# Kernel tuning notes

Measured on AMD Instinct MI355X. Metric: run time of the kernel, lower is better.

## Reference

```python
import jax, jax.numpy as jnp
import numpy as np

B = 4096       # batch
D = 256        # num_features
H = 512        # proposal_hidden_units
K = 10         # mixture_components
C = 64         # context_units
L = 4          # proposal_residual_blocks
S = 10         # num_importance_samples (call default)
HEAD = 3 * K + C
LOG2PI = float(np.log(2.0 * np.pi))


def setup_inputs() -> dict:
    key = jax.random.key(0)
    ks = jax.random.split(key, 10)
    x = jax.random.normal(ks[0], (B, D), jnp.float32)
    observed_mask = (jax.random.uniform(ks[1], (B, D)) < 0.5).astype(jnp.float32)
    s_in = 1.0 / np.sqrt(2 * D)
    s_h = 1.0 / np.sqrt(H)
    W_in = (jax.random.normal(ks[2], (2 * D, H), jnp.float32) * s_in)
    b_in = jnp.zeros((H,), jnp.float32)
    W1 = jax.random.normal(ks[3], (L, H, H), jnp.float32) * s_h
    b1 = jnp.zeros((L, H), jnp.float32)
    W2 = jax.random.normal(ks[4], (L, H, H), jnp.float32) * s_h
    b2 = jnp.zeros((L, H), jnp.float32)
    W_fin = jax.random.normal(ks[5], (H, D * HEAD), jnp.float32) * s_h
    b_fin = jnp.zeros((D * HEAD,), jnp.float32)
    return {
        "x": x, "observed_mask": observed_mask,
        "W_in": W_in, "b_in": b_in,
        "W1": W1, "b1": b1, "W2": W2, "b2": b2,
        "W_fin": W_fin, "b_fin": b_fin,
        "num_importance_samples": S,
    }


def _proposal_params(x_o, observed_mask, W_in, b_in, W1, b1, W2, b2, W_fin, b_fin):
    # Residual MLP proposal network on [x_o, observed_mask].
    h = jnp.concatenate([x_o, observed_mask], axis=-1) @ W_in + b_in  # [B, H]
    for l in range(L):
        r = jax.nn.relu(h) @ W1[l] + b1[l]
        r = jax.nn.relu(r) @ W2[l] + b2[l]
        h = h + r
    out = (h @ W_fin + b_fin).reshape(h.shape[0], D, HEAD)  # [B, D, 3K+C]
    logits = out[..., :K]
    means = out[..., K:2 * K]
    scales = jax.nn.softplus(out[..., 2 * K:3 * K]) + 1e-3
    return logits, means, scales


def reference(x, observed_mask, W_in, b_in, W1, b1, W2, b2, W_fin, b_fin,
              num_importance_samples):
    query = 1.0 - observed_mask
    x_o = x * observed_mask
    x_u = x * query

    logits, means, scales = _proposal_params(
        x_o, observed_mask, W_in, b_in, W1, b1, W2, b2, W_fin, b_fin)

    # Per-feature mixture-of-Gaussians log-likelihood of x_u, masked by query.
    log_w = jax.nn.log_softmax(logits, axis=-1)               # [B, D, K]
    z = (x_u[..., None] - means) / scales
    comp_ll = -0.5 * z * z - jnp.log(scales) - 0.5 * LOG2PI   # [B, D, K]
    proposal_ll = jax.scipy.special.logsumexp(log_w + comp_ll, axis=-1) * query

    # Samples (stop_gradient in the original).
    skey = jax.random.key(1234)
    kc, kn = jax.random.split(skey)
    comp = jax.random.categorical(kc, logits, axis=-1,
                                  shape=(num_importance_samples,) + logits.shape[:2])  # [S, B, D]
    mu = jnp.take_along_axis(means[None], comp[..., None], axis=-1)[..., 0]    # [S, B, D]
    sg = jnp.take_along_axis(scales[None], comp[..., None], axis=-1)[..., 0]   # [S, B, D]
    eps = jax.random.normal(kn, comp.shape, jnp.float32)
    samples = mu + sg * eps                                   # [S, B, D]
    samples = jnp.transpose(samples, (1, 0, 2))               # [B, S, D]
    samples = jax.lax.stop_gradient(samples) * query[:, None, :]
    # call() multiplies by query twice (before and after selected_features block)
    proposal_samples = samples * query[:, None, :]

    proposal_mean = jnp.sum(jax.nn.softmax(logits, axis=-1) * means, axis=-1) * query
    proposal_mean = proposal_mean * query  # second masking, as in call()

    return proposal_ll, proposal_samples, proposal_mean
```

## Files before the change

### kernel.cpp

```cpp
#include <hip/hip_runtime.h>
#include <cstdint>

#define B 4096
#define D 256
#define H 512
#define K 10
#define NL 4
#define S 10
#define NOUT 30
#define HEADW 94
#define ND (B*D)
#define NFIN 7680
#define NLOG 2560
#define NMS  5120

typedef __bf16 bf16x8 __attribute__((ext_vector_type(8)));
typedef float  f32x16 __attribute__((ext_vector_type(16)));

__host__ __device__ inline void threefry2x32(uint32_t k0, uint32_t k1,
                                             uint32_t x0, uint32_t x1,
                                             uint32_t& o0, uint32_t& o1) {
  uint32_t ks2 = k0 ^ k1 ^ 0x1BD11BDAu;
#define TF_ROT(x, r) (((x) << (r)) | ((x) >> (32 - (r))))
#define TF_RND(r) { x0 += x1; x1 = TF_ROT(x1, r); x1 ^= x0; }
  x0 += k0; x1 += k1;
  TF_RND(13) TF_RND(15) TF_RND(26) TF_RND(6)
  x0 += k1; x1 += ks2 + 1u;
  TF_RND(17) TF_RND(29) TF_RND(16) TF_RND(24)
  x0 += ks2; x1 += k0 + 2u;
  TF_RND(13) TF_RND(15) TF_RND(26) TF_RND(6)
  x0 += k0; x1 += k1 + 3u;
  TF_RND(17) TF_RND(29) TF_RND(16) TF_RND(24)
  x0 += k1; x1 += ks2 + 4u;
  TF_RND(13) TF_RND(15) TF_RND(26) TF_RND(6)
  x0 += ks2; x1 += k0 + 5u;
  o0 = x0; o1 = x1;
#undef TF_RND
#undef TF_ROT
}

__device__ __forceinline__ uint32_t rb32(uint32_t k0, uint32_t k1, uint32_t idx) {
  uint32_t a, b;
  threefry2x32(k0, k1, 0u, idx, a, b);
  return a ^ b;
}

__device__ __forceinline__ float u01_from_bits(uint32_t bits) {
  return __uint_as_float((bits >> 9) | 0x3f800000u) - 1.0f;
}

__device__ __forceinline__ float erfinv_f32(float x) {
  float w = -log1pf(-x * x);
  float p;
  if (w < 5.0f) {
    w = w - 2.5f;
    p = 2.81022636e-08f;
    p = fmaf(p, w, 3.43273939e-07f);
    p = fmaf(p, w, -3.5233877e-06f);
    p = fmaf(p, w, -4.39150654e-06f);
    p = fmaf(p, w, 0.00021858087f);
    p = fmaf(p, w, -0.00125372503f);
    p = fmaf(p, w, -0.00417768164f);
    p = fmaf(p, w, 0.246640727f);
    p = fmaf(p, w, 1.50140941f);
  } else {
    w = sqrtf(w) - 3.0f;
    p = -0.000200214257f;
    p = fmaf(p, w, 0.000100950558f);
    p = fmaf(p, w, 0.00134934322f);
    p = fmaf(p, w, -0.00367342844f);
    p = fmaf(p, w, 0.00573950773f);
    p = fmaf(p, w, -0.0076224613f);
    p = fmaf(p, w, 0.00943887047f);
    p = fmaf(p, w, 1.00167406f);
    p = fmaf(p, w, 2.83297682f);
  }
  return p * x;
}

__device__ __forceinline__ unsigned short bf16_rne(float x) {
  uint32_t u = __float_as_uint(x);
  uint32_t r = u + 0x7fffu + ((u >> 16) & 1u);
  return (unsigned short)(r >> 16);
}

__device__ __forceinline__ void split2(float x, short& hi, short& lo) {
  unsigned short hb = bf16_rne(x);
  float hf = __uint_as_float((uint32_t)hb << 16);
  hi = (short)hb;
  lo = (short)bf16_rne(x - hf);
}

__device__ __forceinline__ void gload16(const void* g, void* l) {
  __builtin_amdgcn_global_load_lds(
      (const __attribute__((address_space(1))) void*)g,
      (__attribute__((address_space(3))) void*)l, 16, 0, 0);
}

__global__ __launch_bounds__(256) void prep_kernel(const float* __restrict__ x,
                                                   const float* __restrict__ mask,
                                                   float* __restrict__ xcat) {
  int i = blockIdx.x * 256 + threadIdx.x;
  if (i >= B * 2 * D) return;
  int b = i >> 9, c = i & 511;
  float v = (c < D) ? x[b * D + c] * mask[b * D + c] : mask[b * D + (c - D)];
  xcat[i] = v;
}

__global__ __launch_bounds__(256) void wgatherL(const float* __restrict__ Wf,
                                                float* __restrict__ wsgL) {
  int c = blockIdx.x * 256 + threadIdx.x;
  int k = blockIdx.y;
  int dd = c / K, j = c - dd * K;
  wsgL[(size_t)k * NLOG + c] = Wf[(size_t)k * (D * HEADW) + dd * HEADW + j];
}

__global__ __launch_bounds__(256) void wsplit_ms(const float* __restrict__ Wf,
                                                 short* __restrict__ whi,
                                                 short* __restrict__ wlo) {
  __shared__ float tile[32][33];
  int n0 = blockIdx.x * 32, k0 = blockIdx.y * 32;
  int tx = threadIdx.x & 31, ty = threadIdx.x >> 5;
#pragma unroll
  for (int r = 0; r < 4; ++r) {
    int k = k0 + ty + r * 8;
    int n = n0 + tx;
    int dd = n / 20, j = n - dd * 20;
    tile[ty + r * 8][tx] = Wf[(size_t)k * (D * HEADW) + dd * HEADW + 10 + j];
  }
  __syncthreads();
#pragma unroll
  for (int r = 0; r < 4; ++r) {
    int n = n0 + ty + r * 8;
    int k = k0 + tx;
    float v = tile[tx][ty + r * 8];
    short hb, lb;
    split2(v, hb, lb);
    int nb = n >> 7, nl = n & 127;
    int kc = k >> 5, sub = (k >> 4) & 1, kh = (k >> 3) & 1, e = k & 7;
    size_t idx = ((((size_t)(nb * 16 + kc) * 4 + sub * 2 + kh) * 128 + nl) * 8) + e;
    whi[idx] = hb;
    wlo[idx] = lb;
  }
}

template <int RELU, int RES>
__global__ __launch_bounds__(256) void gemm_trunk(const float* __restrict__ A,
                                                  const float* __restrict__ W,
                                                  const float* __restrict__ bias,
                                                  const float* res, float* C) {
  __shared__ float As[64 * 68];
  __shared__ float Ws[64 * 64];
  const int tid = threadIdx.x;
  const int lane = tid & 63, wid = tid >> 6;
  const int tx = tid & 15, ty = tid >> 4;
  const int bm = blockIdx.y * 64, bn = blockIdx.x * 64;
  const int ls = tid & 15, lm = tid >> 4;

  float acc[4][4] = {};

  for (int k0 = 0; k0 < H; k0 += 64) {
#pragma unroll
    for (int c = wid; c < 16; c += 4) {
      gload16(W + (size_t)(k0 + c * 4 + (lane >> 4)) * H + bn + (lane & 15) * 4,
              Ws + c * 256 + lane * 4);
    }
#pragma unroll
    for (int r = 0; r < 4; ++r) {
      int m = lm + 16 * r;
      float4 f = *(const float4*)(A + (size_t)(bm + m) * H + k0 + 4 * ls);
      if (RELU) {
        f.x = fmaxf(f.x, 0.0f); f.y = fmaxf(f.y, 0.0f);
        f.z = fmaxf(f.z, 0.0f); f.w = fmaxf(f.w, 0.0f);
      }
      As[(4 * ls + 0) * 68 + m] = f.x;
      As[(4 * ls + 1) * 68 + m] = f.y;
      As[(4 * ls + 2) * 68 + m] = f.z;
      As[(4 * ls + 3) * 68 + m] = f.w;
    }
    __syncthreads();
#pragma unroll
    for (int kk = 0; kk < 64; ++kk) {
      float4 a4 = *(const float4*)(As + kk * 68 + ty * 4);
      float4 b4 = *(const float4*)(Ws + kk * 64 + tx * 4);
      float a[4] = {a4.x, a4.y, a4.z, a4.w};
      float b[4] = {b4.x, b4.y, b4.z, b4.w};
#pragma unroll
      for (int i = 0; i < 4; ++i)
#pragma unroll
        for (int j = 0; j < 4; ++j) acc[i][j] = fmaf(a[i], b[j], acc[i][j]);
    }
    __syncthreads();
  }
#pragma unroll
  for (int i = 0; i < 4; ++i) {
    int row = bm + ty * 4 + i;
#pragma unroll
    for (int j = 0; j < 4; ++j) {
      int col = bn + tx * 4 + j;
      float v = acc[i][j] + bias[col];
      if (RES) v = res[(size_t)row * H + col] + v;
      C[(size_t)row * H + col] = v;
    }
  }
}

__global__ __launch_bounds__(256) void gemm_head(const float* __restrict__ A,
                                                 const float* __restrict__ Wg,
                                                 const short* __restrict__ Bh,
                                                 const short* __restrict__ Bl,
                                                 const float* __restrict__ bf,
                                                 const float* __restrict__ msk,
                                                 float* __restrict__ headout) {
  __shared__ __align__(16) float smem[8448];
  const int tid = threadIdx.x;
  const int lane = tid & 63, wid = tid >> 6;
  const int bm = blockIdx.y * 128;

  if (blockIdx.x < 20) {
    float* As = smem;
    float* Ws = smem + 4352;
    const int tx = tid & 15, ty = tid >> 4;
    const int bn = blockIdx.x * 128;
    const int ls = tid & 7, lm = tid >> 3;

    float acc[8][8] = {};

    for (int k0 = 0; k0 < H; k0 += 32) {
#pragma unroll
      for (int c = wid; c < 16; c += 4) {
        gload16(Wg + (size_t)(k0 + c * 2 + (lane >> 5)) * NLOG + bn + (lane & 31) * 4,
                Ws + c * 256 + lane * 4);
      }
#pragma unroll
      for (int r = 0; r < 4; ++r) {
        int m = lm + 32 * r;
        float4 f = *(const float4*)(A + (size_t)(bm + m) * H + k0 + 4 * ls);
        As[(4 * ls + 0) * 136 + m] = f.x;
        As[(4 * ls + 1) * 136 + m] = f.y;
        As[(4 * ls + 2) * 136 + m] = f.z;
        As[(4 * ls + 3) * 136 + m] = f.w;
      }
      __syncthreads();
#pragma unroll
      for (int kk = 0; kk < 32; ++kk) {
        float a[8], b[8];
        *(float4*)(a + 0) = *(const float4*)(As + kk * 136 + ty * 8);
        *(float4*)(a + 4) = *(const float4*)(As + kk * 136 + ty * 8 + 4);
        *(float4*)(b + 0) = *(const float4*)(Ws + kk * 128 + tx * 4);
        *(float4*)(b + 4) = *(const float4*)(Ws + kk * 128 + 64 + tx * 4);
#pragma unroll
        for (int i = 0; i < 8; ++i)
#pragma unroll
          for (int j = 0; j < 8; ++j) acc[i][j] = fmaf(a[i], b[j], acc[i][j]);
      }
      __syncthreads();
    }
#pragma unroll
    for (int i = 0; i < 8; ++i) {
      int row = bm + ty * 8 + i;
#pragma unroll
      for (int j = 0; j < 8; ++j) {
        int c = bn + ((j < 4) ? (tx * 4 + j) : (64 + tx * 4 + (j - 4)));
        int dd = c / K, jj = c - dd * K;
        if (msk[(size_t)row * D + dd] != 0.0f) continue;
        float v = acc[i][j] + bf[dd * HEADW + jj];
        headout[(size_t)row * NFIN + dd * NOUT + jj] = v;
      }
    }
  } else {
    short* lds = (short*)smem;
    const int wm = wid >> 1, wn = wid & 1;
    const int nb = blockIdx.x - 20;
    const int ls = tid & 7, lm = tid >> 3;

    short* ldsAh = lds;
    short* ldsAl = lds + 4096;
    short* ldsBh = lds + 8192;
    short* ldsBl = lds + 12288;

    const short* gBh = Bh + (size_t)nb * 65536;
    const short* gBl = Bl + (size_t)nb * 65536;

    f32x16 acc[2][2];
#pragma unroll
    for (int mt = 0; mt < 2; ++mt)
#pragma unroll
      for (int nt = 0; nt < 2; ++nt)
#pragma unroll
        for (int i = 0; i < 16; ++i) acc[mt][nt][i] = 0.0f;

    for (int kc = 0; kc < 16; ++kc) {
      const short* cBh = gBh + kc * 4096;
      const short* cBl = gBl + kc * 4096;
#pragma unroll
      for (int c = wid; c < 8; c += 4) {
        gload16(cBh + c * 512 + lane * 8, ldsBh + c * 512);
        gload16(cBl + c * 512 + lane * 8, ldsBl + c * 512);
      }
      int k0 = kc * 32;
#pragma unroll
      for (int r = 0; r < 4; ++r) {
        int m = lm + 32 * r;
        float4 f = *(const float4*)(A + (size_t)(bm + m) * H + k0 + 4 * ls);
        short4 h4, l4;
        split2(f.x, h4.x, l4.x); split2(f.y, h4.y, l4.y);
        split2(f.z, h4.z, l4.z); split2(f.w, h4.w, l4.w);
        int off = ((((ls >> 2) * 2 + ((ls >> 1) & 1)) * 128 + m) * 8) + (ls & 1) * 4;
        *(short4*)(ldsAh + off) = h4;
        *(short4*)(ldsAl + off) = l4;
      }
      __syncthreads();
#pragma unroll
      for (int sub = 0; sub < 2; ++sub) {
        bf16x8 ah[2], al[2], bh[2], bl[2];
#pragma unroll
        for (int mt = 0; mt < 2; ++mt) {
          int r = wm * 64 + mt * 32 + (lane & 31);
          int off = ((sub * 2 + (lane >> 5)) * 128 + r) * 8;
          ah[mt] = *(const bf16x8*)(ldsAh + off);
          al[mt] = *(const bf16x8*)(ldsAl + off);
        }
#pragma unroll
        for (int nt = 0; nt < 2; ++nt) {
          int r = wn * 64 + nt * 32 + (lane & 31);
          int off = ((sub * 2 + (lane >> 5)) * 128 + r) * 8;
          bh[nt] = *(const bf16x8*)(ldsBh + off);
          bl[nt] = *(const bf16x8*)(ldsBl + off);
        }
#pragma unroll
        for (int mt = 0; mt < 2; ++mt)
#pragma unroll
          for (int nt = 0; nt < 2; ++nt) {
            acc[mt][nt] = __builtin_amdgcn_mfma_f32_32x32x16_bf16(ah[mt], bh[nt], acc[mt][nt], 0, 0, 0);
            acc[mt][nt] = __builtin_amdgcn_mfma_f32_32x32x16_bf16(ah[mt], bl[nt], acc[mt][nt], 0, 0, 0);
            acc[mt][nt] = __builtin_amdgcn_mfma_f32_32x32x16_bf16(al[mt], bh[nt], acc[mt][nt], 0, 0, 0);
          }
      }
      __syncthreads();
    }

#pragma unroll
    for (int mt = 0; mt < 2; ++mt)
#pragma unroll
      for (int nt = 0; nt < 2; ++nt) {
        int col = nb * 128 + wn * 64 + nt * 32 + (lane & 31);
        int rbase = bm + wm * 64 + mt * 32 + 4 * (lane >> 5);
        int dd = col / 20, j = col - dd * 20;
#pragma unroll
        for (int reg = 0; reg < 16; ++reg) {
          int row = rbase + (reg & 3) + 8 * (reg >> 2);
          if (msk[(size_t)row * D + dd] != 0.0f) continue;
          float v = acc[mt][nt][reg] + bf[dd * HEADW + 10 + j];
          if (j >= 10) v = (fmaxf(v, 0.0f) + log1pf(expf(-fabsf(v)))) + 0.001f;
          headout[(size_t)row * NFIN + dd * NOUT + 10 + j] = v;
        }
      }
  }
}

__global__ __launch_bounds__(256) void init_counter(int* counter) {
  if (threadIdx.x == 0 && blockIdx.x == 0) *counter = 0;
}

__global__ __launch_bounds__(256) void compact_zero(const float* __restrict__ mask,
                                                    float* __restrict__ out_ll,
                                                    float* __restrict__ out_s,
                                                    float* __restrict__ out_mean,
                                                    int* __restrict__ list,
                                                    int* __restrict__ counter) {
  int idx = blockIdx.x * 256 + threadIdx.x;
  if (idx >= ND) return;
  if (mask[idx] != 0.0f) {
    int b = idx >> 8, d = idx & (D - 1);
    out_ll[idx] = 0.0f;
    out_mean[idx] = 0.0f;
#pragma unroll
    for (int s = 0; s < S; ++s) out_s[((size_t)b * S + s) * D + d] = 0.0f;
  } else {
    int pos = atomicAdd(counter, 1);
    list[pos] = idx;
  }
}

__global__ __launch_bounds__(256) void fused_tail(const float* __restrict__ head,
                                                  const float* __restrict__ x,
                                                  const float* __restrict__ mask,
                                                  const int* __restrict__ list,
                                                  const int* __restrict__ counter,
                                                  float* __restrict__ out_ll,
                                                  float* __restrict__ out_s,
                                                  float* __restrict__ out_mean,
                                                  uint32_t kc0, uint32_t kc1,
                                                  uint32_t kn0, uint32_t kn1) {
  int i = blockIdx.x * 256 + threadIdx.x;
  if (i >= *counter) return;
  int idx = list[i];
  int b = idx >> 8, d = idx & (D - 1);
  const float* hp = head + (size_t)idx * NOUT;
  float lg[K], mn[K], sc[K];
#pragma unroll
  for (int k = 0; k < K; ++k) { lg[k] = hp[k]; mn[k] = hp[K + k]; sc[k] = hp[2 * K + k]; }
  float q = 1.0f - mask[idx];
  float xu = x[idx] * q;
  float m = lg[0];
#pragma unroll
  for (int k = 1; k < K; ++k) m = fmaxf(m, lg[k]);
  float e[K];
  float sum = 0.0f;
#pragma unroll
  for (int k = 0; k < K; ++k) { e[k] = expf(lg[k] - m); sum += e[k]; }
  float lse = logf(sum);
  float a[K];
  float amax = -3.402823466e38f;
#pragma unroll
  for (int k = 0; k < K; ++k) {
    float z = (xu - mn[k]) / sc[k];
    float cll = -0.5f * z * z - logf(sc[k]) - 0.9189385332046727f;
    float lw = (lg[k] - m) - lse;
    a[k] = lw + cll;
    amax = fmaxf(amax, a[k]);
  }
  float s2 = 0.0f;
#pragma unroll
  for (int k = 0; k < K; ++k) s2 += expf(a[k] - amax);
  out_ll[idx] = (logf(s2) + amax) * q;
  float pm = 0.0f;
#pragma unroll
  for (int k = 0; k < K; ++k) pm += (e[k] / sum) * mn[k];
  out_mean[idx] = pm * q;
  float inv_e[K];
#pragma unroll
  for (int k = 0; k < K; ++k) inv_e[k] = 1.0f / e[k];
  for (int s = 0; s < S; ++s) {
    uint32_t t32 = (uint32_t)s * (uint32_t)ND + (uint32_t)idx;
    uint32_t base = t32 * (uint32_t)K;
    int best = 0;
    float rbest = 3.402823466e38f;
#pragma unroll
    for (int k = 0; k < K; ++k) {
      uint32_t bits = rb32(kc0, kc1, base + (uint32_t)k);
      float u = u01_from_bits(bits);
      float wv = -__log2f(u);
      float r = wv * inv_e[k];
      if (r < rbest) { rbest = r; best = k; }
    }
    uint32_t ebits = rb32(kn0, kn1, t32);
    float f = u01_from_bits(ebits);
    float r2 = f * 2.0f + (-0.99999994f);
    r2 = fmaxf(r2, -0.99999994f);
    float eps = 1.4142135623730951f * erfinv_f32(r2);
    out_s[((size_t)b * S + s) * D + d] = (mn[best] + sc[best] * eps) * q;
  }
}

extern "C" void kernel_launch(void* const* d_in, const int* in_sizes, int n_in,
                              void* d_out, int out_size, void* d_ws, size_t ws_size,
                              hipStream_t stream) {
  const float* x    = (const float*)d_in[0];
  const float* mask = (const float*)d_in[1];
  const float* W_in = (const float*)d_in[2];
  const float* b_in = (const float*)d_in[3];
  const float* W1   = (const float*)d_in[4];
  const float* b1   = (const float*)d_in[5];
  const float* W2   = (const float*)d_in[6];
  const float* b2   = (const float*)d_in[7];
  const float* Wf   = (const float*)d_in[8];
  const float* bf   = (const float*)d_in[9];

  char* w = (char*)d_ws;
  float* head   = (float*)w;
  float* xcat   = head;
  float* t      = head;
  float* h      = (float*)(w + 125829120);
  float* wsgL   = (float*)(w + 134217728);
  int*   list   = (int*)(w + 134217728);
  short* wms_h  = (short*)(w + 139460608);
  short* wms_l  = (short*)(w + 144703488);
  int*   counter = (int*)(w + 149946368);

  float* out_ll   = (float*)d_out;
  float* out_s    = out_ll + (size_t)ND;
  float* out_mean = out_s + (size_t)ND * S;

  wgatherL<<<dim3(NLOG / 256, 512), 256, 0, stream>>>(Wf, wsgL);
  wsplit_ms<<<dim3(NMS / 32, 512 / 32), 256, 0, stream>>>(Wf, wms_h, wms_l);

  prep_kernel<<<(B * 2 * D) / 256, 256, 0, stream>>>(x, mask, xcat);

  dim3 gtr(H / 64, B / 64);
  gemm_trunk<0, 0><<<gtr, 256, 0, stream>>>(xcat, W_in, b_in, nullptr, h);
  for (int l = 0; l < NL; ++l) {
    gemm_trunk<1, 0><<<gtr, 256, 0, stream>>>(h, W1 + (size_t)l * H * H,
                                              b1 + (size_t)l * H, nullptr, t);
    gemm_trunk<1, 1><<<gtr, 256, 0, stream>>>(t, W2 + (size_t)l * H * H,
                                              b2 + (size_t)l * H, h, h);
  }

  gemm_head<<<dim3(60, B / 128), 256, 0, stream>>>(h, wsgL, wms_h, wms_l, bf,
                                                   mask, head);

  init_counter<<<1, 256, 0, stream>>>(counter);
  compact_zero<<<ND / 256, 256, 0, stream>>>(mask, out_ll, out_s, out_mean,
                                             list, counter);

  uint32_t kc0, kc1, kn0, kn1;
  threefry2x32(0u, 1234u, 0u, 0u, kc0, kc1);
  threefry2x32(0u, 1234u, 0u, 1u, kn0, kn1);
  fused_tail<<<ND / 256, 256, 0, stream>>>(head, x, mask, list, counter,
                                           out_ll, out_s, out_mean,
                                           kc0, kc1, kn0, kn1);
}
```

Measured before the change: 1.314 ms.

## Double-buffer LDS staging in MFMA head GEMM and drop mask-based store skipping

The bf16-split MFMA path of the head GEMM now double-buffers its LDS tiles, staging chunk kc+1 while computing chunk kc with a single barrier per iteration, and uses a simpler A-tile layout with packed 128-bit stores. The aim is to hide global-load and split latency behind MFMA work. Shared memory doubles to 64KB per block, which may lower occupancy. The per-element mask check before writing head outputs is also removed, so every head value is written, trading more stores for less branching and fewer mask loads.

```diff
diff --git a/kernel.cpp b/kernel.cpp
--- a/kernel.cpp
+++ b/kernel.cpp
@@ -91,6 +91,10 @@
   lo = (short)bf16_rne(x - hf);
 }
 
+__device__ __forceinline__ uint32_t pk2(short a, short b) {
+  return (uint32_t)(uint16_t)a | ((uint32_t)(uint16_t)b << 16);
+}
+
 __device__ __forceinline__ void gload16(const void* g, void* l) {
   __builtin_amdgcn_global_load_lds(
       (const __attribute__((address_space(1))) void*)g,
@@ -205,14 +209,41 @@
   }
 }
 
+__device__ __forceinline__ void stage_ms(short* ls0, const float* Ab,
+                                         const short* gBh, const short* gBl,
+                                         int kc, int tid) {
+  const short* cBh = gBh + kc * 4096;
+  const short* cBl = gBl + kc * 4096;
+  gload16(cBh + tid * 8,        ls0 + 8192 + tid * 8);
+  gload16(cBh + 2048 + tid * 8, ls0 + 10240 + tid * 8);
+  gload16(cBl + tid * 8,        ls0 + 12288 + tid * 8);
+  gload16(cBl + 2048 + tid * 8, ls0 + 14336 + tid * 8);
+#pragma unroll
+  for (int p = 0; p < 2; ++p) {
+    int u = tid + p * 256;
+    int slot = u >> 7, row = u & 127;
+    const float* ap = Ab + (size_t)row * 512 + kc * 32 + slot * 8;
+    float4 f0 = *(const float4*)ap;
+    float4 f1 = *(const float4*)(ap + 4);
+    short h0,h1,h2,h3,h4,h5,h6,h7, l0,l1,l2,l3,l4,l5,l6,l7;
+    split2(f0.x, h0, l0); split2(f0.y, h1, l1);
+    split2(f0.z, h2, l2); split2(f0.w, h3, l3);
+    split2(f1.x, h4, l4); split2(f1.y, h5, l5);
+    split2(f1.z, h6, l6); split2(f1.w, h7, l7);
+    uint4 hv = { pk2(h0,h1), pk2(h2,h3), pk2(h4,h5), pk2(h6,h7) };
+    uint4 lv = { pk2(l0,l1), pk2(l2,l3), pk2(l4,l5), pk2(l6,l7) };
+    *(uint4*)(ls0 + u * 8)        = hv;
+    *(uint4*)(ls0 + 4096 + u * 8) = lv;
+  }
+}
+
 __global__ __launch_bounds__(256) void gemm_head(const float* __restrict__ A,
                                                  const float* __restrict__ Wg,
                                                  const short* __restrict__ Bh,
                                                  const short* __restrict__ Bl,
                                                  const float* __restrict__ bf,
-                                                 const float* __restrict__ msk,
                                                  float* __restrict__ headout) {
-  __shared__ __align__(16) float smem[8448];
+  __shared__ __align__(16) float smem[16384];
   const int tid = threadIdx.x;
   const int lane = tid & 63, wid = tid >> 6;
   const int bm = blockIdx.y * 128;
@@ -263,7 +294,6 @@
       for (int j = 0; j < 8; ++j) {
         int c = bn + ((j < 4) ? (tx * 4 + j) : (64 + tx * 4 + (j - 4)));
         int dd = c / K, jj = c - dd * K;
-        if (msk[(size_t)row * D + dd] != 0.0f) continue;
         float v = acc[i][j] + bf[dd * HEADW + jj];
         headout[(size_t)row * NFIN + dd * NOUT + jj] = v;
       }
@@ -272,15 +302,10 @@
     short* lds = (short*)smem;
     const int wm = wid >> 1, wn = wid & 1;
     const int nb = blockIdx.x - 20;
-    const int ls = tid & 7, lm = tid >> 3;
-
-    short* ldsAh = lds;
-    short* ldsAl = lds + 4096;
-    short* ldsBh = lds + 8192;
-    short* ldsBl = lds + 12288;
 
     const short* gBh = Bh + (size_t)nb * 65536;
     const short* gBl = Bl + (size_t)nb * 65536;
+    const float* Ab = A + (size_t)bm * 512;
 
     f32x16 acc[2][2];
 #pragma unroll
@@ -290,27 +315,15 @@
 #pragma unroll
         for (int i = 0; i < 16; ++i) acc[mt][nt][i] = 0.0f;
 
+    stage_ms(lds, Ab, gBh, gBl, 0, tid);
+    int cur = 0;
     for (int kc = 0; kc < 16; ++kc) {
-      const short* cBh = gBh + kc * 4096;
-      const short* cBl = gBl + kc * 4096;
-#pragma unroll
-      for (int c = wid; c < 8; c += 4) {
-        gload16(cBh + c * 512 + lane * 8, ldsBh + c * 512);
-        gload16(cBl + c * 512 + lane * 8, ldsBl + c * 512);
-      }
-      int k0 = kc * 32;
-#pragma unroll
-      for (int r = 0; r < 4; ++r) {
-        int m = lm + 32 * r;
-        float4 f = *(const float4*)(A + (size_t)(bm + m) * H + k0 + 4 * ls);
-        short4 h4, l4;
-        split2(f.x, h4.x, l4.x); split2(f.y, h4.y, l4.y);
-        split2(f.z, h4.z, l4.z); split2(f.w, h4.w, l4.w);
-        int off = ((((ls >> 2) * 2 + ((ls >> 1) & 1)) * 128 + m) * 8) + (ls & 1) * 4;
-        *(short4*)(ldsAh + off) = h4;
-        *(short4*)(ldsAl + off) = l4;
-      }
       __syncthreads();
+      if (kc < 15) stage_ms(lds + (cur ^ 1) * 16384, Ab, gBh, gBl, kc + 1, tid);
+      const short* lsAh = lds + cur * 16384;
+      const short* lsAl = lsAh + 4096;
+      const short* lsBh = lsAh + 8192;
+      const short* lsBl = lsAh + 12288;
 #pragma unroll
       for (int sub = 0; sub < 2; ++sub) {
         bf16x8 ah[2], al[2], bh[2], bl[2];
@@ -318,15 +331,15 @@
         for (int mt = 0; mt < 2; ++mt) {
           int r = wm * 64 + mt * 32 + (lane & 31);
           int off = ((sub * 2 + (lane >> 5)) * 128 + r) * 8;
-          ah[mt] = *(const bf16x8*)(ldsAh + off);
-          al[mt] = *(const bf16x8*)(ldsAl + off);
+          ah[mt] = *(const bf16x8*)(lsAh + off);
+          al[mt] = *(const bf16x8*)(lsAl + off);
         }
 #pragma unroll
         for (int nt = 0; nt < 2; ++nt) {
           int r = wn * 64 + nt * 32 + (lane & 31);
           int off = ((sub * 2 + (lane >> 5)) * 128 + r) * 8;
-          bh[nt] = *(const bf16x8*)(ldsBh + off);
-          bl[nt] = *(const bf16x8*)(ldsBl + off);
+          bh[nt] = *(const bf16x8*)(lsBh + off);
+          bl[nt] = *(const bf16x8*)(lsBl + off);
         }
 #pragma unroll
         for (int mt = 0; mt < 2; ++mt)
@@ -337,7 +350,7 @@
             acc[mt][nt] = __builtin_amdgcn_mfma_f32_32x32x16_bf16(al[mt], bh[nt], acc[mt][nt], 0, 0, 0);
           }
       }
-      __syncthreads();
+      cur ^= 1;
     }
 
 #pragma unroll
@@ -350,7 +363,6 @@
 #pragma unroll
         for (int reg = 0; reg < 16; ++reg) {
           int row = rbase + (reg & 3) + 8 * (reg >> 2);
-          if (msk[(size_t)row * D + dd] != 0.0f) continue;
           float v = acc[mt][nt][reg] + bf[dd * HEADW + 10 + j];
           if (j >= 10) v = (fmaxf(v, 0.0f) + log1pf(expf(-fabsf(v)))) + 0.001f;
           headout[(size_t)row * NFIN + dd * NOUT + 10 + j] = v;
@@ -498,7 +510,7 @@
   }
 
   gemm_head<<<dim3(60, B / 128), 256, 0, stream>>>(h, wsgL, wms_h, wms_l, bf,
-                                                   mask, head);
+                                                   head);
 
   init_counter<<<1, 256, 0, stream>>>(counter);
   compact_zero<<<ND / 256, 256, 0, stream>>>(mask, out_ll, out_s, out_mean,
```

New measurement: 1.369 ms. +4.2%, slower.
